# Optimization experiments

Measured on AMD Instinct MI355X. Metric: run time of the kernel, lower is better.

Reference implementation:

```python
import jax, jax.numpy as jnp
import numpy as np

B, S, D, H = 16, 512, 768, 12
HD = D // H          # head dim 64
L = 512              # att_span = pos_ebd_size
SCALE_FACTOR = 3.0   # c2c + c2p + p2c


def setup_inputs() -> dict:
    key = jax.random.key(0)
    ks = jax.random.split(key, 10)
    std = 0.02
    ids = jnp.arange(S)
    relative_pos = (ids[:, None] - ids[None, :]).astype(jnp.int32)  # [S,S]
    return {
        "q": jax.random.normal(ks[0], (B, S, D), jnp.float32),
        "k": jax.random.normal(ks[1], (B, S, D), jnp.float32),
        "v": jax.random.normal(ks[2], (B, S, D), jnp.float32),
        "rel_embeddings": jax.random.normal(ks[3], (2 * L, D), jnp.float32),
        "Wq": jax.random.normal(ks[4], (D, D), jnp.float32) * std,
        "bq": jnp.zeros((D,), jnp.float32),
        "Wk": jax.random.normal(ks[5], (D, D), jnp.float32) * std,
        "bk": jnp.zeros((D,), jnp.float32),
        "Wv": jax.random.normal(ks[6], (D, D), jnp.float32) * std,
        "bv": jnp.zeros((D,), jnp.float32),
        "relative_pos": relative_pos,
    }


def reference(q, k, v, rel_embeddings, Wq, bq, Wk, bk, Wv, bv, relative_pos):
    # projections + split heads: [B,S,D] -> [B,H,S,HD]
    def split(x):
        return x.reshape(B, S, H, HD).transpose(0, 2, 1, 3)

    Q = split(q @ Wq + bq)
    K = split(k @ Wk + bk)
    V = split(v @ Wv + bv)

    scale = jnp.sqrt(jnp.asarray(HD * SCALE_FACTOR, Q.dtype))
    scores = jnp.einsum('bhqd,bhkd->bhqk', Q, K) / scale  # c2c

    # shared positional projections (share_att_key=True): [2L,H,HD] -> [H,2L,HD]
    pos_k = (rel_embeddings @ Wk + bk).reshape(2 * L, H, HD).transpose(1, 0, 2)
    pos_q = (rel_embeddings @ Wq + bq).reshape(2 * L, H, HD).transpose(1, 0, 2)

    # c2p: bmm then gather along relative-position axis
    c2p_att = jnp.einsum('bhqd,hpd->bhqp', Q, pos_k)          # [B,H,S,2L]
    c2p_idx = jnp.clip(relative_pos + L, 0, 2 * L - 1)        # [S,S]
    c2p = jnp.take_along_axis(
        c2p_att, jnp.broadcast_to(c2p_idx[None, None], (B, H, S, S)), axis=-1)

    # p2c: bmm on keys, gather with -rel_pos, then transpose last two dims
    p2c_att = jnp.einsum('bhkd,hpd->bhkp', K, pos_q)          # [B,H,S,2L]
    p2c_idx = jnp.clip(-relative_pos + L, 0, 2 * L - 1)       # [S,S]
    p2c = jnp.take_along_axis(
        p2c_att, jnp.broadcast_to(p2c_idx[None, None], (B, H, S, S)), axis=-1)
    p2c = jnp.swapaxes(p2c, -1, -2)

    scores = scores + (c2p + p2c) / scale
    probs = jax.nn.softmax(scores, axis=-1)
    ctx = jnp.einsum('bhqk,bhkd->bqhd', probs, V).reshape(B, S, D)
    return ctx
```

## Files before the change

### kernel.cpp

```cpp
#include <hip/hip_runtime.h>


typedef _Float16 f16;
typedef f16 f16x4 __attribute__((ext_vector_type(4)));
typedef f16 f16x8 __attribute__((ext_vector_type(8)));
typedef __fp16 fp16x2 __attribute__((ext_vector_type(2)));
typedef float f32x4 __attribute__((ext_vector_type(4)));

#define D_ 768

__device__ __forceinline__ int swz(int r, int c) { return r * 64 + (c ^ ((r & 7) << 3)); }

__device__ __forceinline__ f32x4 mfma16(f16x8 a, f16x8 b, f32x4 c) {
  return __builtin_amdgcn_mfma_f32_16x16x32_f16(a, b, c, 0, 0, 0);
}

__device__ __forceinline__ f16x4 pack4(float a, float b, float c, float d) {
  fp16x2 lo = __builtin_amdgcn_cvt_pkrtz(a, b);
  fp16x2 hi = __builtin_amdgcn_cvt_pkrtz(c, d);
  f16x4 r;
  r[0] = (f16)lo[0]; r[1] = (f16)lo[1]; r[2] = (f16)hi[0]; r[3] = (f16)hi[1];
  return r;
}

__device__ __forceinline__ void gll16(const f16* g, f16* l) {
  __builtin_amdgcn_global_load_lds((const __attribute__((address_space(1))) void*)g,
                                   (__attribute__((address_space(3))) void*)l, 16, 0, 0);
}

__global__ __launch_bounds__(256) void wtk3(const float* __restrict__ W0, const float* __restrict__ W1,
                                            const float* __restrict__ W2, f16* __restrict__ T0,
                                            f16* __restrict__ T1, f16* __restrict__ T2) {
  __shared__ float t[32][33];
  int z = blockIdx.z;
  const float* W = z == 0 ? W0 : z == 1 ? W1 : W2;
  f16* Wt = z == 0 ? T0 : z == 1 ? T1 : T2;
  int tx = threadIdx.x, ty = threadIdx.y;
  int k0 = blockIdx.x * 32, n0 = blockIdx.y * 32;
  for (int i = ty; i < 32; i += 8) t[i][tx] = W[(k0 + i) * D_ + n0 + tx];
  __syncthreads();
  for (int i = ty; i < 32; i += 8) Wt[(n0 + i) * D_ + k0 + tx] = (f16)t[tx][i];
}

__global__ __launch_bounds__(256) void gemm_all(
    const float* __restrict__ Aq, const float* __restrict__ Ak, const float* __restrict__ Av,
    const float* __restrict__ rel,
    const f16* __restrict__ Wtq, const f16* __restrict__ Wtk, const f16* __restrict__ Wtv,
    const float* __restrict__ bq, const float* __restrict__ bk, const float* __restrict__ bv,
    f16* __restrict__ Qh, f16* __restrict__ Kh, f16* __restrict__ VhT,
    f16* __restrict__ pk, f16* __restrict__ pq) {
  int z = blockIdx.z;
  if (z >= 3 && blockIdx.x >= 8) return;
  __shared__ f16 As[128 * 64];
  __shared__ f16 Bs[128 * 64];
  const float* A; const f16* Wt; const float* bias; f16* out; int mode;
  switch (z) {
    case 0: A = Aq; Wt = Wtq; bias = bq; out = Qh; mode = 0; break;
    case 1: A = Ak; Wt = Wtk; bias = bk; out = Kh; mode = 0; break;
    case 2: A = Av; Wt = Wtv; bias = bv; out = VhT; mode = 2; break;
    case 3: A = rel; Wt = Wtk; bias = bk; out = pk; mode = 1; break;
    default: A = rel; Wt = Wtq; bias = bq; out = pq; mode = 1; break;
  }
  int tid = threadIdx.x, lane = tid & 63, wid = tid >> 6;
  int g4 = lane >> 4, l16 = lane & 15;
  int m0 = blockIdx.x * 128, n0 = blockIdx.y * 128;
  int wr = wid >> 1, wc = wid & 1;
  f32x4 acc[4][4] = {};
  float4 pfA[8];

  auto issueA = [&](int k0) {
#pragma unroll
    for (int i = 0; i < 8; i++) {
      int s = tid + i * 256, r = s >> 4, c = (s & 15) * 4;
      pfA[i] = *(const float4*)(A + (m0 + r) * D_ + k0 + c);
    }
  };

  issueA(0);
  for (int kb = 0; kb < 12; kb++) {
    int k0 = kb * 64;
    __syncthreads();
#pragma unroll
    for (int i = 0; i < 4; i++) {
      int s = tid + i * 256, r = s >> 3, c = (s & 7) * 8;
      int csw = c ^ ((r & 7) << 3);
      gll16(Wt + (n0 + r) * D_ + k0 + csw, &Bs[s * 8]);
    }
#pragma unroll
    for (int i = 0; i < 8; i++) {
      int s = tid + i * 256, r = s >> 4, c = (s & 15) * 4;
      float4 x = pfA[i];
      f16x4 hv; hv[0] = (f16)x.x; hv[1] = (f16)x.y; hv[2] = (f16)x.z; hv[3] = (f16)x.w;
      *(f16x4*)&As[swz(r, c)] = hv;
    }
    if (kb < 11) issueA(k0 + 64);
    __syncthreads();
#pragma unroll
    for (int ks = 0; ks < 2; ks++) {
      f16x8 af[4], bf[4];
#pragma unroll
      for (int mi = 0; mi < 4; mi++) af[mi] = *(const f16x8*)&As[swz(wr * 64 + mi * 16 + l16, ks * 32 + g4 * 8)];
#pragma unroll
      for (int ni = 0; ni < 4; ni++) bf[ni] = *(const f16x8*)&Bs[swz(wc * 64 + ni * 16 + l16, ks * 32 + g4 * 8)];
#pragma unroll
      for (int mi = 0; mi < 4; mi++)
#pragma unroll
        for (int ni = 0; ni < 4; ni++) acc[mi][ni] = mfma16(af[mi], bf[ni], acc[mi][ni]);
    }
  }
#pragma unroll
  for (int mi = 0; mi < 4; mi++)
#pragma unroll
    for (int ni = 0; ni < 4; ni++) {
      int mb = m0 + wr * 64 + mi * 16 + g4 * 4;
      int n = n0 + wc * 64 + ni * 16 + l16;
      int h = n >> 6, hd = n & 63;
      if (mode == 2) {
        int b = mb >> 9, s = mb & 511;
        f16x4 hv;
#pragma unroll
        for (int j = 0; j < 4; j++) hv[j] = (f16)(acc[mi][ni][j] + bias[n]);
        *(f16x4*)&out[(((b * 12 + h) * 64) + hd) * 512 + s] = hv;
      } else {
#pragma unroll
        for (int j = 0; j < 4; j++) {
          int m = mb + j;
          float v = acc[mi][ni][j] + bias[n];
          int idx;
          if (mode == 0) {
            int b = m >> 9, s = m & 511;
            idx = (((b * 12 + h) * 512) + s) * 64 + hd;
          } else {
            idx = ((h * 1024) + m) * 64 + hd;
          }
          out[idx] = (f16)v;
        }
      }
    }
}

__global__ __launch_bounds__(256, 2) void attn(const f16* __restrict__ Qh, const f16* __restrict__ Kh,
                                               const f16* __restrict__ VhT, const f16* __restrict__ posk,
                                               const f16* __restrict__ posq, float* __restrict__ out) {
  __shared__ f16 Ks_[64 * 64];
  __shared__ f16 Vts[64 * 64];
  __shared__ f16 Bband[128 * 64];
  __shared__ f16 bsA[64 * 64];
  __shared__ f16 bs2[64 * 64];

  int tid = threadIdx.x, lane = tid & 63, wid = tid >> 6;
  int g4 = lane >> 4, l16 = lane & 15;
  int flat = blockIdx.x;
  int work = (flat & 7) * 192 + (flat >> 3);
  int q0 = (work & 7) * 64;
  int hb = work >> 3;
  int h = hb % 12, b = hb / 12;

  const f16* Qg = Qh + (b * 12 + h) * 512 * 64;
  const f16* Kg = Kh + (b * 12 + h) * 512 * 64;
  const f16* Vg = VhT + (b * 12 + h) * 64 * 512;
  const f16* PKg = posk + h * 1024 * 64;
  const f16* PQg = posq + h * 1024 * 64;

  int qrow = wid * 16 + l16;
  f16x8 qf[2];
#pragma unroll
  for (int ks = 0; ks < 2; ks++) qf[ks] = *(const f16x8*)(Qg + (q0 + qrow) * 64 + ks * 32 + g4 * 8);

  f16x8 pfK[2], pfV[2], pfC[4], pfP[4];

  auto issue = [&](int kb) {
    int k0 = kb * 64, pbase = q0 - k0 + 449;
#pragma unroll
    for (int i = 0; i < 2; i++) {
      int s = tid + i * 256, r = s >> 3, c = (s & 7) * 8;
      pfK[i] = *(const f16x8*)(Kg + (k0 + r) * 64 + c);
      pfV[i] = *(const f16x8*)(Vg + r * 512 + k0 + c);
    }
#pragma unroll
    for (int i = 0; i < 4; i++) {
      int s = tid + i * 256, r = s >> 3, c = (s & 7) * 8;
      int prow = pbase + r;
      prow = prow > 1023 ? 1023 : prow;
      pfC[i] = *(const f16x8*)(PKg + prow * 64 + c);
      pfP[i] = *(const f16x8*)(PQg + prow * 64 + c);
    }
  };
  auto commitKVC = [&]() {
#pragma unroll
    for (int i = 0; i < 2; i++) {
      int s = tid + i * 256, r = s >> 3, c = (s & 7) * 8;
      *(f16x8*)&Ks_[swz(r, c)] = pfK[i];
      *(f16x8*)&Vts[swz(r, c)] = pfV[i];
    }
#pragma unroll
    for (int i = 0; i < 4; i++) {
      int s = tid + i * 256, r = s >> 3, c = (s & 7) * 8;
      *(f16x8*)&Bband[swz(r, c)] = pfC[i];
    }
  };
  auto commitP = [&]() {
#pragma unroll
    for (int i = 0; i < 4; i++) {
      int s = tid + i * 256, r = s >> 3, c = (s & 7) * 8;
      *(f16x8*)&Bband[swz(r, c)] = pfP[i];
    }
  };

  float mx = -1e30f, lpart = 0.f;
  f32x4 ctx[4] = {};
  const float scale2 = 0.07216878364870323f * 1.4426950408889634f;

  issue(0);
  for (int kb = 0; kb < 8; kb++) {
    commitKVC();
    __syncthreads();

    f16x8 kfw[2], kf[2][4], vf[2][4];
#pragma unroll
    for (int ks = 0; ks < 2; ks++) {
      kfw[ks] = *(const f16x8*)&Ks_[swz(qrow, ks * 32 + g4 * 8)];
#pragma unroll
      for (int ni = 0; ni < 4; ni++) {
        kf[ks][ni] = *(const f16x8*)&Ks_[swz(ni * 16 + l16, ks * 32 + g4 * 8)];
        vf[ks][ni] = *(const f16x8*)&Vts[swz(ni * 16 + l16, ks * 32 + g4 * 8)];
      }
    }
    __builtin_amdgcn_s_setprio(1);
    f32x4 sc[4] = {};
#pragma unroll
    for (int ks = 0; ks < 2; ks++)
#pragma unroll
      for (int ni = 0; ni < 4; ni++) sc[ni] = mfma16(kf[ks][ni], qf[ks], sc[ni]);

#pragma unroll
    for (int t = 0; t < 5; t++) {
      int mi = wid + t;
      f32x4 a2 = {};
#pragma unroll
      for (int ks = 0; ks < 2; ks++) {
        f16x8 bp = *(const f16x8*)&Bband[swz(mi * 16 + l16, ks * 32 + g4 * 8)];
        a2 = mfma16(bp, qf[ks], a2);
      }
      int plocb = mi * 16 + g4 * 4;
#pragma unroll
      for (int j = 0; j < 4; j++) {
        int kk = qrow - (plocb + j) + 63;
        if (kk >= 0 && kk < 64) bsA[swz(qrow, kk)] = (f16)a2[j];
      }
    }
    __builtin_amdgcn_s_setprio(0);
    __syncthreads();
    commitP();
    __syncthreads();

    __builtin_amdgcn_s_setprio(1);
#pragma unroll
    for (int t = 0; t < 5; t++) {
      int nb = 3 - wid + t;
      f32x4 a2 = {};
#pragma unroll
      for (int ks = 0; ks < 2; ks++) {
        f16x8 bq_ = *(const f16x8*)&Bband[swz(nb * 16 + l16, ks * 32 + g4 * 8)];
        a2 = mfma16(kfw[ks], bq_, a2);
      }
#pragma unroll
      for (int j = 0; j < 4; j++) {
        int kk = wid * 16 + g4 * 4 + j;
        int qq = nb * 16 + l16 + kk - 63;
        if (qq >= 0 && qq < 64) bs2[swz(qq, kk)] = (f16)a2[j];
      }
    }
    __builtin_amdgcn_s_setprio(0);
    __syncthreads();
    if (kb < 7) issue(kb + 1);

    f16x4 pa4[4], pc4[4];
#pragma unroll
    for (int ni = 0; ni < 4; ni++) {
      int kb4 = ni * 16 + g4 * 4;
      pa4[ni] = *(const f16x4*)&bsA[swz(qrow, kb4)];
      pc4[ni] = *(const f16x4*)&bs2[swz(qrow, kb4)];
    }
    float mt = -1e30f;
#pragma unroll
    for (int ni = 0; ni < 4; ni++)
#pragma unroll
      for (int j = 0; j < 4; j++) {
        float v = (sc[ni][j] + (float)pa4[ni][j] + (float)pc4[ni][j]) * scale2;
        sc[ni][j] = v;
        mt = fmaxf(mt, v);
      }
    if (!__all(mt <= mx + 6.0f)) {
      float m2 = fmaxf(mt, __shfl_xor(mt, 16, 64));
      m2 = fmaxf(m2, __shfl_xor(m2, 32, 64));
      float corr = __builtin_amdgcn_exp2f(mx - m2);
      mx = m2;
      lpart *= corr;
#pragma unroll
      for (int mi = 0; mi < 4; mi++) ctx[mi] *= corr;
    }
    float rs = 0.f;
#pragma unroll
    for (int ni = 0; ni < 4; ni++) {
      float p0 = __builtin_amdgcn_exp2f(sc[ni][0] - mx);
      float p1 = __builtin_amdgcn_exp2f(sc[ni][1] - mx);
      float p2 = __builtin_amdgcn_exp2f(sc[ni][2] - mx);
      float p3 = __builtin_amdgcn_exp2f(sc[ni][3] - mx);
      rs += (p0 + p1) + (p2 + p3);
      *(f16x4*)&bsA[swz(qrow, ni * 16 + g4 * 4)] = pack4(p0, p1, p2, p3);
    }
    lpart += rs;

    f16x8 pa[2];
#pragma unroll
    for (int ks = 0; ks < 2; ks++) pa[ks] = *(const f16x8*)&bsA[swz(qrow, ks * 32 + g4 * 8)];
    __builtin_amdgcn_s_setprio(1);
#pragma unroll
    for (int mi = 0; mi < 4; mi++)
#pragma unroll
      for (int ks = 0; ks < 2; ks++) ctx[mi] = mfma16(vf[ks][mi], pa[ks], ctx[mi]);
    __builtin_amdgcn_s_setprio(0);
  }
  float ls = lpart;
  ls += __shfl_xor(ls, 16, 64);
  ls += __shfl_xor(ls, 32, 64);
  float inv_l = 1.0f / ls;
#pragma unroll
  for (int mi = 0; mi < 4; mi++) {
    float4 o;
    o.x = ctx[mi][0] * inv_l;
    o.y = ctx[mi][1] * inv_l;
    o.z = ctx[mi][2] * inv_l;
    o.w = ctx[mi][3] * inv_l;
    *(float4*)&out[(b * 512 + q0 + qrow) * 768 + h * 64 + mi * 16 + g4 * 4] = o;
  }
}

extern "C" void kernel_launch(void* const* d_in, const int* in_sizes, int n_in,
                              void* d_out, int out_size, void* d_ws, size_t ws_size,
                              hipStream_t stream) {
  const float* q = (const float*)d_in[0];
  const float* k = (const float*)d_in[1];
  const float* v = (const float*)d_in[2];
  const float* rel = (const float*)d_in[3];
  const float* Wq = (const float*)d_in[4];
  const float* bq = (const float*)d_in[5];
  const float* Wk = (const float*)d_in[6];
  const float* bk = (const float*)d_in[7];
  const float* Wv = (const float*)d_in[8];
  const float* bv = (const float*)d_in[9];
  float* out = (float*)d_out;

  f16* ws = (f16*)d_ws;
  f16* Wtq = ws;
  f16* Wtk = Wtq + 589824;
  f16* Wtv = Wtk + 589824;
  f16* Qh = Wtv + 589824;
  f16* Kh = Qh + 6291456;
  f16* VhT = Kh + 6291456;
  f16* pk = VhT + 6291456;
  f16* pq = pk + 786432;

  wtk3<<<dim3(24, 24, 3), dim3(32, 8), 0, stream>>>(Wq, Wk, Wv, Wtq, Wtk, Wtv);
  gemm_all<<<dim3(64, 6, 5), 256, 0, stream>>>(q, k, v, rel, Wtq, Wtk, Wtv,
                                               bq, bk, bv, Qh, Kh, VhT, pk, pq);
  attn<<<dim3(1536), 256, 0, stream>>>(Qh, Kh, VhT, pk, pq, out);
}
```

Measured before the change: 173.7 us.

## Pre-convert projection inputs to f16 and use async LDS loads in GEMM

The prep kernel now also converts q, k, v and rel_embeddings from fp32 to an f16 staging buffer. A new GEMM kernel then reads these f16 operands with global_load_lds direct-to-LDS loads instead of converting fp32 on the fly. This removes the in-GEMM conversion work and halves the GEMM's A-operand traffic. In exchange it adds a full read-convert-write pass over all inputs and needs a larger workspace, falling back to the old path when the workspace is too small.

```diff
diff --git a/kernel.cpp b/kernel.cpp
--- a/kernel.cpp
+++ b/kernel.cpp
@@ -28,18 +28,117 @@
                                    (__attribute__((address_space(3))) void*)l, 16, 0, 0);
 }
 
-__global__ __launch_bounds__(256) void wtk3(const float* __restrict__ W0, const float* __restrict__ W1,
+__global__ __launch_bounds__(256) void prep(const float* __restrict__ W0, const float* __restrict__ W1,
                                             const float* __restrict__ W2, f16* __restrict__ T0,
-                                            f16* __restrict__ T1, f16* __restrict__ T2) {
+                                            f16* __restrict__ T1, f16* __restrict__ T2,
+                                            const float* __restrict__ q, const float* __restrict__ k,
+                                            const float* __restrict__ v, const float* __restrict__ rel,
+                                            f16* __restrict__ A16) {
   __shared__ float t[32][33];
   int z = blockIdx.z;
-  const float* W = z == 0 ? W0 : z == 1 ? W1 : W2;
-  f16* Wt = z == 0 ? T0 : z == 1 ? T1 : T2;
   int tx = threadIdx.x, ty = threadIdx.y;
-  int k0 = blockIdx.x * 32, n0 = blockIdx.y * 32;
-  for (int i = ty; i < 32; i += 8) t[i][tx] = W[(k0 + i) * D_ + n0 + tx];
-  __syncthreads();
-  for (int i = ty; i < 32; i += 8) Wt[(n0 + i) * D_ + k0 + tx] = (f16)t[tx][i];
+  if (z < 3) {
+    const float* W = z == 0 ? W0 : z == 1 ? W1 : W2;
+    f16* Wt = z == 0 ? T0 : z == 1 ? T1 : T2;
+    int k0 = blockIdx.x * 32, n0 = blockIdx.y * 32;
+    for (int i = ty; i < 32; i += 8) t[i][tx] = W[(k0 + i) * D_ + n0 + tx];
+    __syncthreads();
+    for (int i = ty; i < 32; i += 8) Wt[(n0 + i) * D_ + k0 + tx] = (f16)t[tx][i];
+    return;
+  }
+  const int NQ = 1572864;
+  const int TOT = 3 * NQ + 196608;
+  int tid = ty * 32 + tx;
+  int bid = blockIdx.y * 24 + blockIdx.x;
+  for (int idx = bid * 256 + tid; idx < TOT; idx += 576 * 256) {
+    const float* src; int off;
+    if (idx < NQ) { src = q; off = idx; }
+    else if (idx < 2 * NQ) { src = k; off = idx - NQ; }
+    else if (idx < 3 * NQ) { src = v; off = idx - 2 * NQ; }
+    else { src = rel; off = idx - 3 * NQ; }
+    float4 x = *(const float4*)(src + (size_t)off * 4);
+    f16x4 hv; hv[0] = (f16)x.x; hv[1] = (f16)x.y; hv[2] = (f16)x.z; hv[3] = (f16)x.w;
+    *(f16x4*)&A16[(size_t)idx * 4] = hv;
+  }
+}
+
+__global__ __launch_bounds__(256) void gemm16_all(
+    const f16* __restrict__ A16,
+    const f16* __restrict__ Wtq, const f16* __restrict__ Wtk, const f16* __restrict__ Wtv,
+    const float* __restrict__ bq, const float* __restrict__ bk, const float* __restrict__ bv,
+    f16* __restrict__ Qh, f16* __restrict__ Kh, f16* __restrict__ VhT,
+    f16* __restrict__ pk, f16* __restrict__ pq) {
+  int z = blockIdx.z;
+  if (z >= 3 && blockIdx.x >= 8) return;
+  __shared__ f16 As[128 * 64];
+  __shared__ f16 Bs[128 * 64];
+  const f16* A; const f16* Wt; const float* bias; f16* out; int mode;
+  switch (z) {
+    case 0: A = A16;            Wt = Wtq; bias = bq; out = Qh;  mode = 0; break;
+    case 1: A = A16 + 6291456;  Wt = Wtk; bias = bk; out = Kh;  mode = 0; break;
+    case 2: A = A16 + 12582912; Wt = Wtv; bias = bv; out = VhT; mode = 2; break;
+    case 3: A = A16 + 18874368; Wt = Wtk; bias = bk; out = pk;  mode = 1; break;
+    default: A = A16 + 18874368; Wt = Wtq; bias = bq; out = pq; mode = 1; break;
+  }
+  int tid = threadIdx.x, lane = tid & 63, wid = tid >> 6;
+  int g4 = lane >> 4, l16 = lane & 15;
+  int m0 = blockIdx.x * 128, n0 = blockIdx.y * 128;
+  int wr = wid >> 1, wc = wid & 1;
+  f32x4 acc[4][4] = {};
+
+  for (int kb = 0; kb < 12; kb++) {
+    int k0 = kb * 64;
+    __syncthreads();
+#pragma unroll
+    for (int i = 0; i < 4; i++) {
+      int s = tid + i * 256, r = s >> 3, c = (s & 7) * 8;
+      int csw = c ^ ((r & 7) << 3);
+      gll16(A + (m0 + r) * D_ + k0 + csw, &As[s * 8]);
+      gll16(Wt + (n0 + r) * D_ + k0 + csw, &Bs[s * 8]);
+    }
+    __syncthreads();
+#pragma unroll
+    for (int ks = 0; ks < 2; ks++) {
+      f16x8 af[4], bf[4];
+#pragma unroll
+      for (int mi = 0; mi < 4; mi++) af[mi] = *(const f16x8*)&As[swz(wr * 64 + mi * 16 + l16, ks * 32 + g4 * 8)];
+#pragma unroll
+      for (int ni = 0; ni < 4; ni++) bf[ni] = *(const f16x8*)&Bs[swz(wc * 64 + ni * 16 + l16, ks * 32 + g4 * 8)];
+#pragma unroll
+      for (int mi = 0; mi < 4; mi++)
+#pragma unroll
+        for (int ni = 0; ni < 4; ni++) acc[mi][ni] = mfma16(af[mi], bf[ni], acc[mi][ni]);
+    }
+  }
+#pragma unroll
+  for (int mi = 0; mi < 4; mi++)
+#pragma unroll
+    for (int ni = 0; ni < 4; ni++) {
+      int mb = m0 + wr * 64 + mi * 16 + g4 * 4;
+      int n = n0 + wc * 64 + ni * 16 + l16;
+      int h = n >> 6, hd = n & 63;
+      if (mode == 2) {
+        int b = mb >> 9, s = mb & 511;
+        f16x4 hv;
+#pragma unroll
+        for (int j = 0; j < 4; j++) hv[j] = (f16)(acc[mi][ni][j] + bias[n]);
+        *(f16x4*)&out[(((b * 12 + h) * 64) + hd) * 512 + s] = hv;
+      } else {
+#pragma unroll
+        for (int j = 0; j < 4; j++) {
+          int m = mb + j;
+          float v = acc[mi][ni][j] + bias[n];
+          int idx;
+          if (mode == 0) {
+            int b = m >> 9, s = m & 511;
+            idx = (((b * 12 + h) * 512) + s) * 64 + hd;
+          } else {
+            idx = ((h * 1024) + m) * 64 + hd;
+          }
+          out[idx] = (f16)v;
+        }
+      }
+    }
 }
 
 __global__ __launch_bounds__(256) void gemm_all(
@@ -361,9 +460,19 @@
   f16* VhT = Kh + 6291456;
   f16* pk = VhT + 6291456;
   f16* pq = pk + 786432;
-
-  wtk3<<<dim3(24, 24, 3), dim3(32, 8), 0, stream>>>(Wq, Wk, Wv, Wtq, Wtk, Wtv);
-  gemm_all<<<dim3(64, 6, 5), 256, 0, stream>>>(q, k, v, rel, Wtq, Wtk, Wtv,
-                                               bq, bk, bv, Qh, Kh, VhT, pk, pq);
+  f16* A16 = pq + 786432;
+
+  const size_t need_f16 = 3 * 589824 + 3 * 6291456 + 2 * 786432 + 19660800;
+  bool fast = ws_size >= need_f16 * sizeof(f16);
+
+  prep<<<dim3(24, 24, fast ? 4 : 3), dim3(32, 8), 0, stream>>>(
+      Wq, Wk, Wv, Wtq, Wtk, Wtv, q, k, v, rel, A16);
+  if (fast) {
+    gemm16_all<<<dim3(64, 6, 5), 256, 0, stream>>>(A16, Wtq, Wtk, Wtv,
+                                                   bq, bk, bv, Qh, Kh, VhT, pk, pq);
+  } else {
+    gemm_all<<<dim3(64, 6, 5), 256, 0, stream>>>(q, k, v, rel, Wtq, Wtk, Wtv,
+                                                 bq, bk, bv, Qh, Kh, VhT, pk, pq);
+  }
   attn<<<dim3(1536), 256, 0, stream>>>(Qh, Kh, VhT, pk, pq, out);
 }
```

Result: slower. 177.2 us (+2.0%).
